# Performance work log

Measured on AMD Instinct MI355X. Metric: run time of the kernel, lower is better.

The kernel has to match this reference:

```python
import jax, jax.numpy as jnp
import numpy as np

N = 20000   # nodes
E = 40000   # edges
B = 1000    # graphs
F = 32      # num_features
D = 64      # dim


def setup_inputs() -> dict:
    key = jax.random.key(0)
    ks = jax.random.split(key, 16)
    def g(k, shape, scale=0.05):
        return jax.random.normal(k, shape, jnp.float32) * scale
    return dict(
        x=jax.random.normal(ks[0], (N, F), jnp.float32),
        edge_attr=jax.random.uniform(ks[1], (E, 5), jnp.float32),
        edge_index=jax.random.randint(ks[2], (2, E), 0, N),
        batch=jnp.sort(jax.random.randint(ks[3], (N,), 0, B)),
        W0=g(ks[4], (D, F)), b0=jnp.zeros((D,), jnp.float32),
        We1=g(ks[5], (128, 5)), be1=jnp.zeros((128,), jnp.float32),
        We2=g(ks[6], (D * D, 128), 0.01), be2=jnp.zeros((D * D,), jnp.float32),
        b_conv=jnp.zeros((D,), jnp.float32),
        W_ih=g(ks[7], (3 * D, D)), W_hh=g(ks[8], (3 * D, D)),
        b_ih=jnp.zeros((3 * D,), jnp.float32), b_hh=jnp.zeros((3 * D,), jnp.float32),
        W_ihl=g(ks[9], (4 * D, 2 * D)), W_hhl=g(ks[10], (4 * D, D)),
        b_ihl=jnp.zeros((4 * D,), jnp.float32), b_hhl=jnp.zeros((4 * D,), jnp.float32),
        W1=g(ks[11], (D, 2 * D)), b1=jnp.zeros((D,), jnp.float32),
        W2=g(ks[12], (1, D)), b2=jnp.zeros((1,), jnp.float32),
    )


def reference(x, edge_attr, edge_index, batch, W0, b0, We1, be1, We2, be2,
              b_conv, W_ih, W_hh, b_ih, b_hh, W_ihl, W_hhl, b_ihl, b_hhl,
              W1, b1, W2, b2):
    src, dst = edge_index[0], edge_index[1]
    # lin0 + relu
    out = jax.nn.relu(x @ W0.T + b0)            # [N, D]
    h = out                                     # GRU hidden
    # edge-conditioned weights (identical each iteration in the original)
    We = jax.nn.relu(edge_attr @ We1.T + be1) @ We2.T + be2
    We = We.reshape(E, D, D)                    # [E, in, out]
    deg = jnp.maximum(jax.ops.segment_sum(jnp.ones((E,), out.dtype), dst, N), 1.0)[:, None]
    for _ in range(3):
        msg = jnp.einsum('ei,eio->eo', out[src], We)          # [E, D]
        agg = jax.ops.segment_sum(msg, dst, num_segments=N) / deg
        m = jax.nn.relu(agg + b_conv)
        # GRU cell (gate order r, z, n as in torch)
        gi = m @ W_ih.T + b_ih
        gh = h @ W_hh.T + b_hh
        ir, iz, inn = jnp.split(gi, 3, -1)
        hr, hz, hn = jnp.split(gh, 3, -1)
        r = jax.nn.sigmoid(ir + hr)
        z = jax.nn.sigmoid(iz + hz)
        n = jnp.tanh(inn + r * hn)
        h = (1.0 - z) * n + z * h
        out = h
    # Set2Set pooling (3 processing steps), LSTM gate order i, f, g, o
    q_star = jnp.zeros((B, 2 * D), out.dtype)
    hl = jnp.zeros((B, D), out.dtype)
    cl = jnp.zeros((B, D), out.dtype)
    for _ in range(3):
        gates = q_star @ W_ihl.T + b_ihl + hl @ W_hhl.T + b_hhl
        i_, f_, g_, o_ = jnp.split(gates, 4, -1)
        cl = jax.nn.sigmoid(f_) * cl + jax.nn.sigmoid(i_) * jnp.tanh(g_)
        hl = jax.nn.sigmoid(o_) * jnp.tanh(cl)
        q = hl                                               # [B, D]
        e = jnp.sum(out * q[batch], -1)                      # [N]
        emax = jax.ops.segment_max(e, batch, num_segments=B)
        a = jnp.exp(e - emax[batch])
        a = a / jax.ops.segment_sum(a, batch, num_segments=B)[batch]
        r_ = jax.ops.segment_sum(a[:, None] * out, batch, num_segments=B)
        q_star = jnp.concatenate([q, r_], -1)                # [B, 2D]
    y = jax.nn.relu(q_star @ W1.T + b1)
    pred = (y @ W2.T + b2).reshape(-1)                       # [B]
    return pred
```

## Files before the change

kernel.cpp:

```cpp
#include <hip/hip_runtime.h>

#define NN 20000
#define NE 40000
#define NGR 1000
#define KH 2
#define WTF_BIAS 524288

typedef unsigned short u16;
typedef u16 u16x8 __attribute__((ext_vector_type(8)));
typedef __bf16 bf16x8 __attribute__((ext_vector_type(8)));
typedef float f32x4 __attribute__((ext_vector_type(4)));

union U8 { u16x8 u; bf16x8 b; };

__device__ __forceinline__ u16 f2bf(float f) {
    union { float f; unsigned u; } v; v.f = f;
    unsigned r = v.u + 0x7FFF + ((v.u >> 16) & 1);
    return (u16)(r >> 16);
}
__device__ __forceinline__ float bf2f(u16 h) {
    union { unsigned u; float f; } v; v.u = ((unsigned)h) << 16;
    return v.f;
}
__device__ __forceinline__ float sigmoidf(float x) { return 1.f / (1.f + __expf(-x)); }

__device__ __forceinline__ void gl_lds16(const u16* g, u16* l) {
    __builtin_amdgcn_global_load_lds(
        (const __attribute__((address_space(1))) void*)g,
        (__attribute__((address_space(3))) void*)l, 16, 0, 0);
}

__global__ __launch_bounds__(256) void k_cnt(const int* __restrict__ ei, int* __restrict__ cnt)
{
    for (int e = blockIdx.x * 256 + threadIdx.x; e < NE; e += gridDim.x * 256)
        atomicAdd(&cnt[ei[NE + e]], 1);
}

__global__ __launch_bounds__(1024) void k_scan(const int* __restrict__ cnt,
                                               int* __restrict__ rowptr)
{
    __shared__ int ps[1024];
    int t = threadIdx.x;
    int base = t * 20;
    int loc[20];
    int s = 0;
#pragma unroll
    for (int i = 0; i < 20; ++i) {
        int idx = base + i;
        loc[i] = s;
        s += (idx < NN) ? cnt[idx] : 0;
    }
    ps[t] = s;
    __syncthreads();
    for (int off = 1; off < 1024; off <<= 1) {
        int v = (t >= off) ? ps[t - off] : 0;
        __syncthreads();
        ps[t] += v;
        __syncthreads();
    }
    int ex = (t > 0) ? ps[t - 1] : 0;
#pragma unroll
    for (int i = 0; i < 20; ++i) {
        int idx = base + i;
        if (idx < NN) rowptr[idx] = ex + loc[i];
    }
    if (t == 1023) rowptr[NN] = ps[1023];
}

__global__ __launch_bounds__(256) void k_scatter(const int* __restrict__ ei,
    const int* __restrict__ rowptr, int* __restrict__ cur,
    int* __restrict__ epos, int* __restrict__ srcs)
{
    for (int e = blockIdx.x * 256 + threadIdx.x; e < NE; e += gridDim.x * 256) {
        int d = ei[NE + e];
        int pos = rowptr[d] + atomicAdd(&cur[d], 1);
        epos[e] = pos;
        srcs[pos] = ei[e];
    }
}

__global__ __launch_bounds__(256) void k_pre(
    const float* __restrict__ x, const float* __restrict__ ea,
    const int* __restrict__ batch, const int* __restrict__ epos,
    const float* __restrict__ W0, const float* __restrict__ b0,
    const float* __restrict__ We1, const float* __restrict__ be1,
    const float* __restrict__ We2, const float* __restrict__ be2,
    const float* __restrict__ W_ih, const float* __restrict__ W_hh,
    const float* __restrict__ W_ihl, const float* __restrict__ W_hhl,
    const float* __restrict__ W1,
    float* __restrict__ h, u16* __restrict__ outb, u16* __restrict__ h1,
    u16* __restrict__ WtF, int* __restrict__ gstart, int* __restrict__ gend,
    u16* __restrict__ WgF,
    float* __restrict__ WTihl, float* __restrict__ WThhl, float* __restrict__ WT1)
{
    const int b = blockIdx.x;
    const int t = threadIdx.x;

    if (b < 64) {
        for (int idx = b * 256 + t; idx < 90112; idx += 64 * 256) {
            int i = idx;
            if (i < 32768) {
                int j = i & 7, lane = (i >> 3) & 63;
                int nt = (i >> 9) & 15, ks = i >> 13;
                int o = nt * 16 + (lane & 15);
                int k = ks * 32 + (lane >> 4) * 8 + j;
                float v;
                if (o < 128)      v = (k < 64) ? W_ih[o * 64 + k] : W_hh[o * 64 + k - 64];
                else if (o < 192) v = (k < 64) ? W_ih[o * 64 + k] : 0.f;
                else              v = (k >= 64) ? W_hh[(o - 64) * 64 + k - 64] : 0.f;
                WgF[i] = f2bf(v);
                continue;
            }
            i -= 32768;
            if (i < 32768) { WTihl[i] = W_ihl[(i % 256) * 128 + i / 256]; continue; }
            i -= 32768;
            if (i < 16384) { WThhl[i] = W_hhl[(i % 256) * 64 + i / 256]; continue; }
            i -= 16384;
            WT1[i] = W1[(i % 64) * 128 + i / 64];
        }
        return;
    }
    if (b < 320) {
        int wv = (b - 64) * 4 + (t >> 6);
        int lane = t & 63;
        float w0r[32];
#pragma unroll
        for (int f = 0; f < 32; ++f) w0r[f] = W0[lane * 32 + f];
        float b0v = b0[lane];
        for (int n = wv; n < NN; n += 1024) {
            float xv = (lane < 32) ? x[n * 32 + lane] : 0.f;
            float acc = b0v;
#pragma unroll
            for (int f = 0; f < 32; ++f) acc += __shfl(xv, f, 64) * w0r[f];
            float rv = fmaxf(acc, 0.f);
            h[n * 64 + lane] = rv;
            outb[n * 64 + lane] = f2bf(rv);
        }
        return;
    }
    if (b < 832) {
        for (int idx = (b - 320) * 256 + t; idx < NE * 128; idx += 512 * 256) {
            int e = idx >> 7, k = idx & 127;
            float acc = be1[k];
#pragma unroll
            for (int j = 0; j < 5; ++j)
                acc += ea[e * 5 + j] * We1[k * 5 + j];
            h1[(size_t)epos[e] * 128 + k] = f2bf(fmaxf(acc, 0.f));
        }
        return;
    }
    if (b < 960) {
        for (int idx = (b - 832) * 256 + t; idx < WTF_BIAS + 4096; idx += 128 * 256) {
            float v;
            if (idx < WTF_BIAS) {
                int j = idx & 7, lane = (idx >> 3) & 63;
                int nt = (idx >> 9) & 3, s4 = (idx >> 11) & 3, ch = idx >> 13;
                int o = nt * 16 + (lane & 15);
                int k = s4 * 32 + (lane >> 4) * 8 + j;
                v = We2[(size_t)(ch * 64 + o) * 128 + k];
            } else {
                int bx = idx - WTF_BIAS;
                int j = bx & 7, lane = (bx >> 3) & 63;
                int nt = (bx >> 9) & 3, sb = bx >> 11;
                int o = nt * 16 + (lane & 15);
                int i = sb * 32 + (lane >> 4) * 8 + j;
                v = be2[i * 64 + o];
            }
            WtF[idx] = f2bf(v);
        }
        return;
    }
    {
        for (int idx = (b - 960) * 256 + t; idx < NN; idx += 32 * 256) {
            int bg = batch[idx];
            if (idx == 0 || batch[idx - 1] != bg) gstart[bg] = idx;
            if (idx == NN - 1 || batch[idx + 1] != bg) gend[bg] = idx + 1;
        }
    }
}

__global__ __launch_bounds__(256, 4) void k_msg(
    const u16* __restrict__ outb, const u16* __restrict__ h1,
    const u16* __restrict__ WtF, const int* __restrict__ srcs,
    u16* __restrict__ pbuf)
{
    __shared__ __align__(8) u16 svT[64 * 132];
    __shared__ __align__(16) u16 LB[2 * 4096];
    const int t = threadIdx.x;
    const int eb0 = blockIdx.x * 128;
    const int kh = blockIdx.y;
    const int ohc = (int)blockIdx.z * 2;

#pragma unroll
    for (int r = 0; r < 4; ++r) {
        int cid = t + 256 * r;
        int row = cid >> 3, c8 = cid & 7;
        int e = eb0 + row;
        u16x8 v = {};
        if (e < NE) { int s = srcs[e]; v = *(const u16x8*)(outb + (size_t)s * 64 + c8 * 8); }
        int rs = row ^ (c8 << 2);
#pragma unroll
        for (int j = 0; j < 8; ++j)
            svT[(c8 * 8 + j) * 132 + rs] = v[j];
    }

    const int lane = t & 63, w = t >> 6, r16 = lane & 15, q = lane >> 4;
    const int w32 = w * 32;

    u16x8 h1r[2][4];
#pragma unroll
    for (int sub = 0; sub < 2; ++sub) {
        int e = eb0 + w32 + sub * 16 + r16;
        if (e >= NE) e = NE - 1;
        const u16* hp = h1 + (size_t)e * 128 + q * 8;
#pragma unroll
        for (int s4 = 0; s4 < 4; ++s4)
            h1r[sub][s4] = *(const u16x8*)(hp + s4 * 32);
    }

    f32x4 acc[2][2];
    const f32x4 z4 = {0.f, 0.f, 0.f, 0.f};
#pragma unroll
    for (int sub = 0; sub < 2; ++sub)
#pragma unroll
        for (int nt = 0; nt < 2; ++nt) acc[sub][nt] = z4;

    const int chBase = kh * 32;
    u16* lb0 = &LB[0];
    u16* lb1 = &LB[4096];

    auto STAGE = [&](u16* lb, int ch) {
        const u16* g = WtF + (size_t)ch * 8192 + w * 2048 + ohc * 512 + lane * 8;
        gl_lds16(g,       lb + (2 * w) * 512);
        gl_lds16(g + 512, lb + (2 * w + 1) * 512);
    };
    auto SCALE = [&](f32x4 (&P)[2][2], int ch) {
        int swz = ((ch >> 3) & 7) << 2;
#pragma unroll
        for (int sub = 0; sub < 2; ++sub) {
            int mb = (w32 + sub * 16 + q * 4) ^ swz;
            uint2 rv = *(const uint2*)&svT[ch * 132 + mb];
            union { unsigned u; float f; } c0, c1, c2, c3;
            c0.u = rv.x << 16; c1.u = rv.x & 0xffff0000u;
            c2.u = rv.y << 16; c3.u = rv.y & 0xffff0000u;
#pragma unroll
            for (int nt = 0; nt < 2; ++nt) {
                acc[sub][nt][0] += c0.f * P[sub][nt][0];
                acc[sub][nt][1] += c1.f * P[sub][nt][1];
                acc[sub][nt][2] += c2.f * P[sub][nt][2];
                acc[sub][nt][3] += c3.f * P[sub][nt][3];
            }
        }
    };

    STAGE(lb0, chBase);

#pragma unroll 1
    for (int cc = 0; cc < 32; ++cc) {
        u16* cur = (cc & 1) ? lb1 : lb0;
        u16* nxt = (cc & 1) ? lb0 : lb1;
        if (cc < 31) {
            STAGE(nxt, chBase + cc + 1);
            asm volatile("s_waitcnt vmcnt(2) lgkmcnt(0)" ::: "memory");
        } else {
            asm volatile("s_waitcnt vmcnt(0) lgkmcnt(0)" ::: "memory");
        }
        __builtin_amdgcn_s_barrier();
        asm volatile("" ::: "memory");

        U8 bv[8];
#pragma unroll
        for (int f = 0; f < 8; ++f)
            bv[f].u = *(const u16x8*)(cur + f * 512 + lane * 8);

        if (cc < 31) {
            asm volatile("s_waitcnt lgkmcnt(0)" ::: "memory");
            __builtin_amdgcn_s_barrier();
            asm volatile("" ::: "memory");
        }

        __builtin_amdgcn_s_setprio(1);
        f32x4 P[2][2];
#pragma unroll
        for (int s4 = 0; s4 < 4; ++s4)
#pragma unroll
            for (int sub = 0; sub < 2; ++sub) {
                U8 a; a.u = h1r[sub][s4];
#pragma unroll
                for (int nt = 0; nt < 2; ++nt)
                    P[sub][nt] = __builtin_amdgcn_mfma_f32_16x16x32_bf16(
                        a.b, bv[s4 * 2 + nt].b, (s4 == 0) ? z4 : P[sub][nt], 0, 0, 0);
            }
        __builtin_amdgcn_s_setprio(0);
        SCALE(P, chBase + cc);
    }

    if (kh == KH - 1) {
        U8 bvb[2][2];
#pragma unroll
        for (int sb = 0; sb < 2; ++sb)
#pragma unroll
            for (int nt = 0; nt < 2; ++nt)
                bvb[sb][nt].u = *(const u16x8*)(WtF + WTF_BIAS +
                                                ((sb * 4 + ohc + nt) * 64 + lane) * 8);
#pragma unroll
        for (int sub = 0; sub < 2; ++sub) {
            int m = w32 + sub * 16 + r16;
#pragma unroll
            for (int sb = 0; sb < 2; ++sb) {
                U8 a;
#pragma unroll
                for (int j = 0; j < 8; ++j) {
                    int ch = sb * 32 + q * 8 + j;
                    a.u[j] = svT[ch * 132 + (m ^ (((ch >> 3) & 7) << 2))];
                }
#pragma unroll
                for (int nt = 0; nt < 2; ++nt)
                    acc[sub][nt] = __builtin_amdgcn_mfma_f32_16x16x32_bf16(
                        a.b, bvb[sb][nt].b, acc[sub][nt], 0, 0, 0);
            }
        }
    }

#pragma unroll
    for (int sub = 0; sub < 2; ++sub) {
#pragma unroll
        for (int r = 0; r < 4; ++r) {
            int e = eb0 + w32 + sub * 16 + q * 4 + r;
            if (e >= NE) continue;
            u16* pp = pbuf + (size_t)e * (KH * 64) + kh * 64 + r16;
#pragma unroll
            for (int nt = 0; nt < 2; ++nt)
                pp[(ohc + nt) * 16] = f2bf(acc[sub][nt][r]);
        }
    }
}

__global__ __launch_bounds__(256) void k_gru(float* __restrict__ h, u16* __restrict__ outb,
    const u16* __restrict__ pbuf, const int* __restrict__ rowptr,
    const float* __restrict__ b_conv, const u16* __restrict__ WgF,
    const float* __restrict__ b_ih, const float* __restrict__ b_hh)
{
    __shared__ __align__(16) u16 zA[64 * 132];
    __shared__ float hS[64 * 65];
    const int t = threadIdx.x;
    const int lane = t & 63, w = t >> 6, r16 = lane & 15, q = lane >> 4;
    const int n0 = blockIdx.x * 64;
    const int w16 = w * 16;
    float bcv = b_conv[lane];

#pragma unroll 1
    for (int p = 0; p < 16; ++p) {
        int n = n0 + w16 + p;
        float m = 0.f, hvv = 0.f;
        if (n < NN) {
            int rs = rowptr[n], re = rowptr[n + 1];
            float v = 0.f;
            const u16* pb = pbuf + (size_t)rs * (KH * 64);
            for (int j = rs; j < re; ++j) {
                v += bf2f(pb[lane]) + bf2f(pb[64 + lane]);
                pb += KH * 64;
            }
            m = fmaxf(v / fmaxf((float)(re - rs), 1.f) + bcv, 0.f);
            hvv = h[n * 64 + lane];
        }
        zA[(w16 + p) * 132 + lane] = f2bf(m);
        zA[(w16 + p) * 132 + 64 + lane] = f2bf(hvv);
        hS[(w16 + p) * 65 + lane] = hvv;
    }

    u16x8 afr[4];
#pragma unroll
    for (int ks = 0; ks < 4; ++ks)
        afr[ks] = *(const u16x8*)&zA[(w16 + r16) * 132 + ks * 32 + q * 8];

    f32x4 acc[16];
    const f32x4 z4 = {0.f, 0.f, 0.f, 0.f};
#pragma unroll
    for (int nt = 0; nt < 16; ++nt) acc[nt] = z4;

    U8 bA[4], bB[4];
    auto LDB = [&](U8* dst, int nt) {
#pragma unroll
        for (int ks = 0; ks < 4; ++ks)
            dst[ks].u = *(const u16x8*)(WgF + ((ks * 16 + nt) * 64 + lane) * 8);
    };
    LDB(bA, 0);
#pragma unroll
    for (int nt = 0; nt < 16; ++nt) {
        U8* cur = (nt & 1) ? bB : bA;
        U8* nxt = (nt & 1) ? bA : bB;
        if (nt < 15) LDB(nxt, nt + 1);
        f32x4 c = acc[nt];
#pragma unroll
        for (int ks = 0; ks < 4; ++ks) {
            U8 a; a.u = afr[ks];
            c = __builtin_amdgcn_mfma_f32_16x16x32_bf16(a.b, cur[ks].b, c, 0, 0, 0);
        }
        acc[nt] = c;
    }

#pragma unroll
    for (int reg = 0; reg < 4; ++reg) {
        int nl = w16 + q * 4 + reg;
        int n = n0 + nl;
        if (n >= NN) continue;
#pragma unroll
        for (int dd = 0; dd < 4; ++dd) {
            int d = dd * 16 + r16;
            float rv = acc[dd][reg]      + b_ih[d]       + b_hh[d];
            float zv = acc[4 + dd][reg]  + b_ih[64 + d]  + b_hh[64 + d];
            float iv = acc[8 + dd][reg]  + b_ih[128 + d];
            float hg = acc[12 + dd][reg] + b_hh[128 + d];
            float rr = sigmoidf(rv), zz = sigmoidf(zv);
            float nn = tanhf(iv + rr * hg);
            float hold = hS[nl * 65 + d];
            float hnew = (1.f - zz) * nn + zz * hold;
            h[n * 64 + d] = hnew;
            outb[n * 64 + d] = f2bf(hnew);
        }
    }
}

__global__ __launch_bounds__(256) void k_s2s(const float* __restrict__ h,
    const int* __restrict__ gstart, const int* __restrict__ gend,
    const float* __restrict__ WTihl, const float* __restrict__ WThhl,
    const float* __restrict__ b_ihl, const float* __restrict__ b_hhl,
    const float* __restrict__ WT1, const float* __restrict__ b1,
    const float* __restrict__ W2, const float* __restrict__ b2,
    float* __restrict__ outp)
{
    __shared__ float qs[128];
    __shared__ float hlL[64], clL[64];
    __shared__ float gt[256];
    __shared__ float sm[4], sl[4], sr[4][64];
    const int g = blockIdx.x;
    const int t = threadIdx.x, w = t >> 6, lane = t & 63;
    const int s = gstart[g], e = gend[g];

    if (t < 128) qs[t] = 0.f;
    if (t < 64) { hlL[t] = 0.f; clL[t] = 0.f; }
    __syncthreads();

    for (int step = 0; step < 3; ++step) {
        float ga = b_ihl[t] + b_hhl[t];
#pragma unroll 4
        for (int j = 0; j < 128; ++j)
            ga += qs[j] * WTihl[j * 256 + t];
#pragma unroll 4
        for (int j = 0; j < 64; ++j)
            ga += hlL[j] * WThhl[j * 256 + t];
        gt[t] = ga;
        __syncthreads();
        if (t < 64) {
            float cv = sigmoidf(gt[64 + t]) * clL[t] + sigmoidf(gt[t]) * tanhf(gt[128 + t]);
            float hn = sigmoidf(gt[192 + t]) * tanhf(cv);
            clL[t] = cv; hlL[t] = hn; qs[t] = hn;
        }
        __syncthreads();
        float qv = hlL[lane];
        float M = -3.4e38f, l = 0.f, r = 0.f;
        for (int n = s + w; n < e; n += 4) {
            float hvv = h[n * 64 + lane];
            float p = hvv * qv;
#pragma unroll
            for (int off = 32; off > 0; off >>= 1) p += __shfl_xor(p, off, 64);
            if (p > M) {
                float sc = __expf(M - p);
                l = l * sc + 1.f;
                r = r * sc + hvv;
                M = p;
            } else {
                float pe = __expf(p - M);
                l += pe;
                r += pe * hvv;
            }
        }
        if (lane == 0) { sm[w] = M; sl[w] = l; }
        sr[w][lane] = r;
        __syncthreads();
        if (w == 0) {
            float Mg = fmaxf(fmaxf(sm[0], sm[1]), fmaxf(sm[2], sm[3]));
            float lg = 0.f, rg = 0.f;
#pragma unroll
            for (int wp = 0; wp < 4; ++wp) {
                float sc = __expf(sm[wp] - Mg);
                lg += sl[wp] * sc;
                rg += sr[wp][lane] * sc;
            }
            float inv = (lg > 0.f) ? 1.f / lg : 0.f;
            qs[64 + lane] = rg * inv;
        }
        __syncthreads();
    }
    float acc = 0.f;
#pragma unroll 4
    for (int j = w * 32; j < w * 32 + 32; ++j)
        acc += qs[j] * WT1[j * 64 + lane];
    sr[w][lane] = acc;
    __syncthreads();
    if (w == 0) {
        float y = sr[0][lane] + sr[1][lane] + sr[2][lane] + sr[3][lane] + b1[lane];
        float pr = fmaxf(y, 0.f) * W2[lane];
#pragma unroll
        for (int off = 32; off > 0; off >>= 1) pr += __shfl_xor(pr, off, 64);
        if (lane == 0) outp[g] = pr + b2[0];
    }
}

extern "C" void kernel_launch(void* const* d_in, const int* in_sizes, int n_in,
                              void* d_out, int out_size, void* d_ws, size_t ws_size,
                              hipStream_t stream)
{
    const float* x      = (const float*)d_in[0];
    const float* ea     = (const float*)d_in[1];
    const int*   ei     = (const int*)d_in[2];
    const int*   batch  = (const int*)d_in[3];
    const float* W0     = (const float*)d_in[4];
    const float* b0     = (const float*)d_in[5];
    const float* We1    = (const float*)d_in[6];
    const float* be1    = (const float*)d_in[7];
    const float* We2    = (const float*)d_in[8];
    const float* be2    = (const float*)d_in[9];
    const float* b_conv = (const float*)d_in[10];
    const float* W_ih   = (const float*)d_in[11];
    const float* W_hh   = (const float*)d_in[12];
    const float* b_ih   = (const float*)d_in[13];
    const float* b_hh   = (const float*)d_in[14];
    const float* W_ihl  = (const float*)d_in[15];
    const float* W_hhl  = (const float*)d_in[16];
    const float* b_ihl  = (const float*)d_in[17];
    const float* b_hhl  = (const float*)d_in[18];
    const float* W1     = (const float*)d_in[19];
    const float* b1     = (const float*)d_in[20];
    const float* W2     = (const float*)d_in[21];
    const float* b2     = (const float*)d_in[22];
    float* outp = (float*)d_out;

    char* ws = (char*)d_ws;
    size_t off = 0;
    auto alloc = [&](size_t bytes) -> char* {
        char* p = ws + off;
        off += (bytes + 255) & ~(size_t)255;
        return p;
    };
    u16*   h1     = (u16*)  alloc((size_t)NE * 128 * 2);
    u16*   WtF    = (u16*)  alloc((WTF_BIAS + 4096) * 2);
    u16*   outb   = (u16*)  alloc((size_t)NN * 64 * 2);
    float* h      = (float*)alloc((size_t)NN * 64 * 4);
    u16*   pbuf   = (u16*)  alloc((size_t)NE * KH * 64 * 2);
    int*   rowptr = (int*)  alloc((NN + 1) * 4);
    int*   epos   = (int*)  alloc(NE * 4);
    int*   srcs   = (int*)  alloc(NE * 4);
    int*   cnt    = (int*)  alloc(NN * 4);
    int*   cur    = (int*)  alloc(NN * 4);
    int*   gstart = (int*)  alloc(NGR * 4);
    int*   gend   = (int*)  alloc(NGR * 4);
    u16*   WgF    = (u16*)  alloc(32768 * 2);
    float* WTihl  = (float*)alloc(32768 * 4);
    float* WThhl  = (float*)alloc(16384 * 4);
    float* WT1    = (float*)alloc(8192 * 4);
    if (off > ws_size) return;

    size_t zspan = (size_t)((char*)(gend + NGR) - (char*)cnt);
    hipMemsetAsync(cnt, 0, zspan, stream);

    k_cnt<<<64, 256, 0, stream>>>(ei, cnt);
    k_scan<<<1, 1024, 0, stream>>>(cnt, rowptr);
    k_scatter<<<64, 256, 0, stream>>>(ei, rowptr, cur, epos, srcs);
    k_pre<<<992, 256, 0, stream>>>(x, ea, batch, epos, W0, b0, We1, be1, We2, be2,
                                   W_ih, W_hh, W_ihl, W_hhl, W1,
                                   h, outb, h1, WtF, gstart, gend,
                                   WgF, WTihl, WThhl, WT1);

    dim3 mgrid((NE + 127) / 128, KH, 2);
    for (int it = 0; it < 3; ++it) {
        k_msg<<<mgrid, 256, 0, stream>>>(outb, h1, WtF, srcs, pbuf);
        k_gru<<<313, 256, 0, stream>>>(h, outb, pbuf, rowptr, b_conv,
                                       WgF, b_ih, b_hh);
    }
    k_s2s<<<NGR, 256, 0, stream>>>(h, gstart, gend, WTihl, WThhl, b_ihl, b_hhl,
                                   WT1, b1, W2, b2, outp);
}
```

Before: 423.2 us.

## Fuse message aggregation into k_msg via float atomics, drop per-edge partial buffer

k_msg no longer writes bf16 per-edge partial messages to a pbuf. It pre-reduces consecutive edges that share a destination (edges are CSR-sorted by destination) and atomically adds the sums into an fp32 per-node agg buffer. k_gru reads agg, divides by degree, and zeroes it for the next iteration, which removes the serial per-edge gather loop. This trades the pbuf write/read traffic for global float atomics, whose contention, extra memset size and nondeterministic summation order add cost and variance.

```diff
diff --git a/kernel.cpp b/kernel.cpp
--- a/kernel.cpp
+++ b/kernel.cpp
@@ -69,13 +69,14 @@
 
 __global__ __launch_bounds__(256) void k_scatter(const int* __restrict__ ei,
     const int* __restrict__ rowptr, int* __restrict__ cur,
-    int* __restrict__ epos, int* __restrict__ srcs)
+    int* __restrict__ epos, int* __restrict__ srcs, int* __restrict__ dsts)
 {
     for (int e = blockIdx.x * 256 + threadIdx.x; e < NE; e += gridDim.x * 256) {
         int d = ei[NE + e];
         int pos = rowptr[d] + atomicAdd(&cur[d], 1);
         epos[e] = pos;
         srcs[pos] = ei[e];
+        dsts[pos] = d;
     }
 }
 
@@ -182,7 +183,7 @@
 __global__ __launch_bounds__(256, 4) void k_msg(
     const u16* __restrict__ outb, const u16* __restrict__ h1,
     const u16* __restrict__ WtF, const int* __restrict__ srcs,
-    u16* __restrict__ pbuf)
+    const int* __restrict__ dsts, float* __restrict__ agg)
 {
     __shared__ __align__(8) u16 svT[64 * 132];
     __shared__ __align__(16) u16 LB[2 * 4096];
@@ -324,20 +325,30 @@
 
 #pragma unroll
     for (int sub = 0; sub < 2; ++sub) {
-#pragma unroll
-        for (int r = 0; r < 4; ++r) {
-            int e = eb0 + w32 + sub * 16 + q * 4 + r;
-            if (e >= NE) continue;
-            u16* pp = pbuf + (size_t)e * (KH * 64) + kh * 64 + r16;
-#pragma unroll
-            for (int nt = 0; nt < 2; ++nt)
-                pp[(ohc + nt) * 16] = f2bf(acc[sub][nt][r]);
+        int eb = eb0 + w32 + sub * 16 + q * 4;
+        if (eb >= NE) continue;
+        int d0 = dsts[eb];
+        int d1 = (eb + 1 < NE) ? dsts[eb + 1] : -1;
+        int d2 = (eb + 2 < NE) ? dsts[eb + 2] : -1;
+        int d3 = (eb + 3 < NE) ? dsts[eb + 3] : -1;
+#pragma unroll
+        for (int nt = 0; nt < 2; ++nt) {
+            float* base = agg + (ohc + nt) * 16 + r16;
+            float run = acc[sub][nt][0];
+            int dp = d0;
+            if (d1 == dp) run += acc[sub][nt][1];
+            else { atomicAdd(base + (size_t)dp * 64, run); dp = d1; run = acc[sub][nt][1]; }
+            if (d2 == dp) run += acc[sub][nt][2];
+            else { if (dp >= 0) atomicAdd(base + (size_t)dp * 64, run); dp = d2; run = acc[sub][nt][2]; }
+            if (d3 == dp) run += acc[sub][nt][3];
+            else { if (dp >= 0) atomicAdd(base + (size_t)dp * 64, run); dp = d3; run = acc[sub][nt][3]; }
+            if (dp >= 0) atomicAdd(base + (size_t)dp * 64, run);
         }
     }
 }
 
 __global__ __launch_bounds__(256) void k_gru(float* __restrict__ h, u16* __restrict__ outb,
-    const u16* __restrict__ pbuf, const int* __restrict__ rowptr,
+    float* __restrict__ agg, const int* __restrict__ rowptr,
     const float* __restrict__ b_conv, const u16* __restrict__ WgF,
     const float* __restrict__ b_ih, const float* __restrict__ b_hh)
 {
@@ -349,19 +360,15 @@
     const int w16 = w * 16;
     float bcv = b_conv[lane];
 
-#pragma unroll 1
+#pragma unroll 4
     for (int p = 0; p < 16; ++p) {
         int n = n0 + w16 + p;
         float m = 0.f, hvv = 0.f;
         if (n < NN) {
-            int rs = rowptr[n], re = rowptr[n + 1];
-            float v = 0.f;
-            const u16* pb = pbuf + (size_t)rs * (KH * 64);
-            for (int j = rs; j < re; ++j) {
-                v += bf2f(pb[lane]) + bf2f(pb[64 + lane]);
-                pb += KH * 64;
-            }
-            m = fmaxf(v / fmaxf((float)(re - rs), 1.f) + bcv, 0.f);
+            float av = agg[(size_t)n * 64 + lane];
+            agg[(size_t)n * 64 + lane] = 0.f;
+            float deg = fmaxf((float)(rowptr[n + 1] - rowptr[n]), 1.f);
+            m = fmaxf(av / deg + bcv, 0.f);
             hvv = h[n * 64 + lane];
         }
         zA[(w16 + p) * 132 + lane] = f2bf(m);
@@ -548,26 +555,27 @@
     u16*   WtF    = (u16*)  alloc((WTF_BIAS + 4096) * 2);
     u16*   outb   = (u16*)  alloc((size_t)NN * 64 * 2);
     float* h      = (float*)alloc((size_t)NN * 64 * 4);
-    u16*   pbuf   = (u16*)  alloc((size_t)NE * KH * 64 * 2);
     int*   rowptr = (int*)  alloc((NN + 1) * 4);
     int*   epos   = (int*)  alloc(NE * 4);
     int*   srcs   = (int*)  alloc(NE * 4);
+    int*   dsts   = (int*)  alloc(NE * 4);
     int*   cnt    = (int*)  alloc(NN * 4);
     int*   cur    = (int*)  alloc(NN * 4);
     int*   gstart = (int*)  alloc(NGR * 4);
     int*   gend   = (int*)  alloc(NGR * 4);
+    float* agg    = (float*)alloc((size_t)NN * 64 * 4);
     u16*   WgF    = (u16*)  alloc(32768 * 2);
     float* WTihl  = (float*)alloc(32768 * 4);
     float* WThhl  = (float*)alloc(16384 * 4);
     float* WT1    = (float*)alloc(8192 * 4);
     if (off > ws_size) return;
 
-    size_t zspan = (size_t)((char*)(gend + NGR) - (char*)cnt);
+    size_t zspan = (size_t)((char*)(agg + (size_t)NN * 64) - (char*)cnt);
     hipMemsetAsync(cnt, 0, zspan, stream);
 
     k_cnt<<<64, 256, 0, stream>>>(ei, cnt);
     k_scan<<<1, 1024, 0, stream>>>(cnt, rowptr);
-    k_scatter<<<64, 256, 0, stream>>>(ei, rowptr, cur, epos, srcs);
+    k_scatter<<<64, 256, 0, stream>>>(ei, rowptr, cur, epos, srcs, dsts);
     k_pre<<<992, 256, 0, stream>>>(x, ea, batch, epos, W0, b0, We1, be1, We2, be2,
                                    W_ih, W_hh, W_ihl, W_hhl, W1,
                                    h, outb, h1, WtF, gstart, gend,
@@ -575,8 +583,8 @@
 
     dim3 mgrid((NE + 127) / 128, KH, 2);
     for (int it = 0; it < 3; ++it) {
-        k_msg<<<mgrid, 256, 0, stream>>>(outb, h1, WtF, srcs, pbuf);
-        k_gru<<<313, 256, 0, stream>>>(h, outb, pbuf, rowptr, b_conv,
+        k_msg<<<mgrid, 256, 0, stream>>>(outb, h1, WtF, srcs, dsts, agg);
+        k_gru<<<313, 256, 0, stream>>>(h, outb, agg, rowptr, b_conv,
                                        WgF, b_ih, b_hh);
     }
     k_s2s<<<NGR, 256, 0, stream>>>(h, gstart, gend, WTihl, WThhl, b_ihl, b_hhl,
```

Result: faster. 414.7 us (-2.0%).
